# Optimization experiments

Measured on AMD Instinct MI355X. Metric: run time of the kernel, lower is better.

The kernel has to match this reference:

```python
import jax, jax.numpy as jnp
import numpy as np

B, N, DIM = 64, 512, 256
H, DH = 8, 64
INNER = H * DH
SCALE = DH ** -0.5


def setup_inputs() -> dict:
    key = jax.random.key(0)
    ks = jax.random.split(key, 8)
    x = jax.random.normal(ks[0], (B, N, DIM), dtype=jnp.float32)
    mask = jax.random.bernoulli(ks[1], 0.9, (B, N))
    attn_bias = jax.random.normal(ks[2], (1, H, N, N), dtype=jnp.float32)
    # weights stored [in, out] (torch Linear applies x @ W.T; here W = W_torch.T)
    Wq = jax.random.normal(ks[3], (DIM, INNER), dtype=jnp.float32) * (DIM ** -0.5)
    Wkv = jax.random.normal(ks[4], (DIM, 2 * INNER), dtype=jnp.float32) * (DIM ** -0.5)
    Wo = jax.random.normal(ks[5], (INNER, DIM), dtype=jnp.float32) * (INNER ** -0.5)
    bo = jnp.zeros((DIM,), dtype=jnp.float32)
    # gating linear: torch init is weight=0, bias=1 (gates==1); use small random
    # perturbation around that so the gate path is exercised numerically
    Wg = jax.random.normal(ks[6], (DIM, INNER), dtype=jnp.float32) * 0.02
    bg = jnp.ones((INNER,), dtype=jnp.float32)
    return {"x": x, "mask": mask, "attn_bias": attn_bias,
            "Wq": Wq, "Wkv": Wkv, "Wo": Wo, "bo": bo, "Wg": Wg, "bg": bg}


def reference(x, mask, attn_bias, Wq, Wkv, Wo, bo, Wg, bg):
    b, n, _ = x.shape
    # projections (no bias on q/kv, per nn.Linear(..., bias=False))
    q = x @ Wq                               # [b, n, H*DH]
    kv = x @ Wkv                             # [b, n, 2*H*DH]
    k, v = jnp.split(kv, 2, axis=-1)
    split_heads = lambda t: t.reshape(b, n, H, DH).transpose(0, 2, 1, 3)  # b h n d
    q, k, v = split_heads(q), split_heads(k), split_heads(v)
    dots = jnp.einsum('bhid,bhjd->bhij', q, k) * SCALE + attn_bias
    pair_mask = mask[:, None, :, None] & mask[:, None, None, :]  # [b,1,i,j]
    mask_value = -jnp.finfo(dots.dtype).max
    dots = jnp.where(pair_mask, dots, mask_value)
    attn = jax.nn.softmax(dots, axis=-1)
    out = jnp.einsum('bhij,bhjd->bhid', attn, v)
    out = out.transpose(0, 2, 1, 3).reshape(b, n, INNER)  # b n (h d)
    gates = x @ Wg + bg                      # note: no sigmoid in the original
    out = out * gates
    return out @ Wo + bo
```

## Files before the change

kernel.cpp:

```cpp
#include <hip/hip_runtime.h>
#include <stdint.h>

#define B_    64
#define N_    512
#define DIM_  256
#define H_    8
#define DH_   64
#define INNER_ 512

typedef __attribute__((ext_vector_type(8))) short bf16x8;
typedef __attribute__((ext_vector_type(4))) float f32x4;
typedef __attribute__((ext_vector_type(4))) short s16x4;

typedef const __attribute__((address_space(1))) void* gas_ptr;
typedef __attribute__((address_space(3))) void* las_ptr;

__device__ __forceinline__ short f2bf(float f) {
  unsigned int u = __float_as_uint(f);
  u += 0x7fffu + ((u >> 16) & 1u);
  return (short)(u >> 16);
}
__device__ __forceinline__ float bf2f(short s) {
  return __uint_as_float(((unsigned int)(unsigned short)s) << 16);
}
__device__ __forceinline__ void cp16(const void* g, void* l) {
  __builtin_amdgcn_global_load_lds((gas_ptr)g, (las_ptr)l, 16, 0, 0);
}
__device__ __forceinline__ f32x4 mfma16(bf16x8 a, bf16x8 b, f32x4 c) {
  return __builtin_amdgcn_mfma_f32_16x16x32_bf16(a, b, c, 0, 0, 0);
}

#define PREP_WT1  (2048 * 256)
#define PREP_WOT  (256 * 512)
#define PREP_X    (32768 * 256)
#define PREP_BIAS (8 * 512 * 512)
#define PREP_MASK (64 * 512)
#define PREP_TOT  (PREP_WT1 + PREP_WOT + PREP_X + PREP_BIAS + PREP_MASK)

__global__ void prep_k(const float* __restrict__ x,
                       const float* __restrict__ Wq, const float* __restrict__ Wkv,
                       const float* __restrict__ Wg, const float* __restrict__ Wo,
                       const float* __restrict__ bias, const int* __restrict__ mask,
                       short* __restrict__ Wt1, short* __restrict__ WoT,
                       short* __restrict__ xb, float* __restrict__ biasS,
                       float* __restrict__ maskF)
{
  const int idx = blockIdx.x * 256 + threadIdx.x;
  if (idx < PREP_WT1) {
    const int n = idx >> 8, k = idx & 255;
    float v;
    if (n < 512)        v = Wq[k * 512 + n];
    else if (n < 1536)  v = Wkv[k * 1024 + (n - 512)];
    else                v = Wg[k * 512 + (n - 1536)];
    Wt1[idx] = f2bf(v);
  } else if (idx < PREP_WT1 + PREP_WOT) {
    const int j = idx - PREP_WT1;
    const int n = j >> 9, k = j & 511;
    WoT[j] = f2bf(Wo[k * 256 + n]);
  } else if (idx < PREP_WT1 + PREP_WOT + PREP_X) {
    const int j = idx - (PREP_WT1 + PREP_WOT);
    xb[j] = f2bf(x[j]);
  } else if (idx < PREP_WT1 + PREP_WOT + PREP_X + PREP_BIAS) {
    const int j = idx - (PREP_WT1 + PREP_WOT + PREP_X);
    biasS[j] = bias[j] * 1.4426950408889634f;
  } else if (idx < PREP_TOT) {
    const int j = idx - (PREP_WT1 + PREP_WOT + PREP_X + PREP_BIAS);
    maskF[j] = mask[j] ? 1.0f : 0.0f;
  }
}

__global__ __launch_bounds__(256, 2) void gemm_qkvg(
    const short* __restrict__ X, const short* __restrict__ Wt,
    const float* __restrict__ bg,
    short* __restrict__ Q, short* __restrict__ Kb,
    short* __restrict__ Vt, short* __restrict__ G)
{
  __shared__ __align__(16) short As[128 * 32];
  __shared__ __align__(16) short Bs[128 * 32];
  const int tid = threadIdx.x;
  const int w = tid >> 6, lane = tid & 63;
  const int m = lane & 15, q = lane >> 4;
  const int n0 = blockIdx.x * 128, m0 = blockIdx.y * 128;
  const int region = blockIdx.x >> 2;
  const bool vreg = (region == 2);
  const int ric = lane >> 2, cslot = lane & 3;
  const int csw = cslot ^ ((ric >> 1) & 3);
  const int wr = (w >> 1) * 64, wc = (w & 1) * 64;
  const int rsw = (m >> 1) & 3;
  f32x4 acc[4][4] = {};
  for (int k0 = 0; k0 < DIM_; k0 += 32) {
    __syncthreads();
#pragma unroll
    for (int s = 0; s < 2; ++s) {
      const int rr = w * 32 + s * 16;
      cp16(X  + (size_t)(m0 + rr + ric) * DIM_ + (k0 + csw * 8), &As[rr * 32]);
      cp16(Wt + (size_t)(n0 + rr + ric) * DIM_ + (k0 + csw * 8), &Bs[rr * 32]);
    }
    __syncthreads();
    bf16x8 af[4], bfv[4];
#pragma unroll
    for (int t = 0; t < 4; ++t) {
      af[t]  = *(const bf16x8*)&As[(wr + t * 16 + m) * 32 + ((q ^ rsw) * 8)];
      bfv[t] = *(const bf16x8*)&Bs[(wc + t * 16 + m) * 32 + ((q ^ rsw) * 8)];
    }
    if (vreg) {
#pragma unroll
      for (int ti = 0; ti < 4; ++ti)
#pragma unroll
        for (int tj = 0; tj < 4; ++tj)
          acc[ti][tj] = mfma16(af[ti], bfv[tj], acc[ti][tj]);
    } else {
#pragma unroll
      for (int ti = 0; ti < 4; ++ti)
#pragma unroll
        for (int tj = 0; tj < 4; ++tj)
          acc[ti][tj] = mfma16(bfv[tj], af[ti], acc[ti][tj]);
    }
  }
  if (vreg) {
    const int cb = (n0 & 511) + wc;
#pragma unroll
    for (int ti = 0; ti < 4; ++ti) {
      const int mgb = m0 + wr + ti * 16 + q * 4;
      const int b = mgb >> 9, n = mgb & 511;
#pragma unroll
      for (int tj = 0; tj < 4; ++tj) {
        const int c = cb + tj * 16 + m;
        const int h = c >> 6, d = c & 63;
        s16x4 st;
#pragma unroll
        for (int r = 0; r < 4; ++r) st[r] = f2bf(acc[ti][tj][r]);
        *(s16x4*)&Vt[((size_t)(b * 8 + h) * 64 + d) * 512 + n] = st;
      }
    }
  } else {
#pragma unroll
    for (int ti = 0; ti < 4; ++ti) {
      const int xrow = m0 + wr + ti * 16 + m;
      const int b = xrow >> 9, n = xrow & 511;
#pragma unroll
      for (int tj = 0; tj < 4; ++tj) {
        const int cvec = (n0 & 511) + wc + tj * 16 + q * 4;
        if (region == 3) {
          const f32x4 bg4 = *(const f32x4*)&bg[cvec];
          s16x4 st;
#pragma unroll
          for (int r = 0; r < 4; ++r) st[r] = f2bf(acc[ti][tj][r] + bg4[r]);
          *(s16x4*)&G[(size_t)xrow * 512 + cvec] = st;
        } else {
          const int h = cvec >> 6, d0 = cvec & 63;
          s16x4 st;
#pragma unroll
          for (int r = 0; r < 4; ++r) st[r] = f2bf(acc[ti][tj][r]);
          short* dst = (region == 0) ? Q : Kb;
          *(s16x4*)&dst[((size_t)(b * 8 + h) * 512 + n) * 64 + d0] = st;
        }
      }
    }
  }
}

__global__ __launch_bounds__(256, 4) void attn_k(
    const short* __restrict__ Q, const short* __restrict__ K,
    const short* __restrict__ Vt, const float* __restrict__ biasS,
    const float* __restrict__ maskF, short* __restrict__ G)
{
  __shared__ __align__(16) short Ks[2][32 * 64];
  __shared__ __align__(16) short Vs[2][64 * 32];
  __shared__ __align__(16) short Pall[4][16 * 32];
  const int tid = threadIdx.x;
  const int w = tid >> 6, lane = tid & 63;
  const int m = lane & 15, q = lane >> 4;
  const int m7 = m & 7;
  const int vsw = (m ^ (m >> 2)) & 3;
  const int h = blockIdx.x, iq = blockIdx.y, b = blockIdx.z;
  const int i0w = iq * 128 + w * 32;
  const size_t bh = (size_t)b * 8 + h;
  const short* Qp = Q + (bh * 512 + i0w) * 64;
  const short* Kp = K + bh * 512 * 64;
  const short* Vp = Vt + bh * 64 * 512;
  const float* mkp = maskF + b * 512;
  short* Ps = Pall[w];

  const int srow = lane >> 3;
  const int gchunk = (lane & 7) ^ srow;
  const int vrow = lane >> 2;
  const int gchunkV = (lane & 3) ^ ((vrow ^ (vrow >> 2)) & 3);

  bf16x8 qf[2][2];
#pragma unroll
  for (int it = 0; it < 2; ++it) {
    qf[it][0] = *(const bf16x8*)&Qp[(it * 16 + m) * 64 + q * 8];
    qf[it][1] = *(const bf16x8*)&Qp[(it * 16 + m) * 64 + 32 + q * 8];
  }
  float miF[2];
#pragma unroll
  for (int it = 0; it < 2; ++it) miF[it] = mkp[i0w + it * 16 + m];

  cp16(Kp + (size_t)(w * 8 + srow) * 64 + gchunk * 8, &Ks[0][w * 8 * 64]);
  cp16(Vp + (size_t)(w * 16 + vrow) * 512 + gchunkV * 8, &Vs[0][w * 16 * 32]);

  f32x4 o[2][4] = {};
  float l[2] = {0.f, 0.f};
  __syncthreads();

  const float SCL = 0.125f * 1.4426950408889634f;
  for (int c = 0; c < 16; ++c) {
    const int p = c & 1;
    if (c < 15) {
      const int jn = (c + 1) * 32;
      cp16(Kp + (size_t)(jn + w * 8 + srow) * 64 + gchunk * 8, &Ks[p ^ 1][w * 8 * 64]);
      cp16(Vp + (size_t)(w * 16 + vrow) * 512 + jn + gchunkV * 8, &Vs[p ^ 1][w * 16 * 32]);
    }
    f32x4 mjf[2];
#pragma unroll
    for (int jt = 0; jt < 2; ++jt)
      mjf[jt] = *(const f32x4*)&mkp[c * 32 + jt * 16 + q * 4];

    f32x4 s[2][2];
    __builtin_amdgcn_s_setprio(1);
#pragma unroll
    for (int jt = 0; jt < 2; ++jt) {
      const bf16x8 ka = *(const bf16x8*)&Ks[p][(jt * 16 + m) * 64 + ((q ^ m7) * 8)];
      const bf16x8 kb = *(const bf16x8*)&Ks[p][(jt * 16 + m) * 64 + (((4 + q) ^ m7) * 8)];
#pragma unroll
      for (int it = 0; it < 2; ++it) {
        f32x4 a = {};
        a = mfma16(ka, qf[it][0], a);
        s[it][jt] = mfma16(kb, qf[it][1], a);
      }
    }
    __builtin_amdgcn_s_setprio(0);
#pragma unroll
    for (int it = 0; it < 2; ++it) {
      const float* bp = biasS + ((size_t)h * 512 + i0w + it * 16 + m) * 512 + c * 32;
      f32x4 bv[2];
#pragma unroll
      for (int jt = 0; jt < 2; ++jt)
        bv[jt] = *(const f32x4*)&bp[jt * 16 + q * 4];
#pragma unroll
      for (int jt = 0; jt < 2; ++jt) {
        s16x4 st;
#pragma unroll
        for (int r = 0; r < 4; ++r) {
          const float v = fmaf(s[it][jt][r], SCL, bv[jt][r]);
          float e = exp2f(v) * mjf[jt][r];
          e = (miF[it] != 0.0f) ? e : 1.0f;
          const unsigned u = __float_as_uint(e);
          st[r] = (short)(u >> 16);
          l[it] += __uint_as_float(u & 0xffff0000u);
        }
        *(s16x4*)&Ps[m * 32 + (((jt * 2 + (q >> 1)) ^ vsw) * 8) + (q & 1) * 4] = st;
      }
      const bf16x8 pa = *(const bf16x8*)&Ps[m * 32 + ((q ^ vsw) * 8)];
      __builtin_amdgcn_s_setprio(1);
#pragma unroll
      for (int dt = 0; dt < 4; ++dt) {
        const bf16x8 va = *(const bf16x8*)&Vs[p][(dt * 16 + m) * 32 + ((q ^ vsw) * 8)];
        o[it][dt] = mfma16(pa, va, o[it][dt]);
      }
      __builtin_amdgcn_s_setprio(0);
    }
    __syncthreads();
  }

#pragma unroll
  for (int it = 0; it < 2; ++it) {
    float t = l[it];
    t += __shfl_xor(t, 16, 64);
    t += __shfl_xor(t, 32, 64);
    l[it] = 1.0f / t;
  }
  const int colb = h * 64;
#pragma unroll
  for (int it = 0; it < 2; ++it) {
    float lr[4];
#pragma unroll
    for (int r = 0; r < 4; ++r) lr[r] = __shfl(l[it], q * 4 + r, 16);
#pragma unroll
    for (int dt = 0; dt < 4; ++dt)
#pragma unroll
      for (int r = 0; r < 4; ++r) {
        const int row = i0w + it * 16 + q * 4 + r;
        const size_t addr = ((size_t)b * 512 + row) * 512 + colb + dt * 16 + m;
        const float gate = bf2f(G[addr]);
        G[addr] = f2bf(o[it][dt][r] * lr[r] * gate);
      }
  }
}

__global__ __launch_bounds__(256, 2) void gemm_og(
    const short* __restrict__ A, const short* __restrict__ Bt,
    const float* __restrict__ bo, float* __restrict__ out)
{
  __shared__ __align__(16) short As[64 * 32];
  __shared__ __align__(16) short Bs[128 * 32];
  const int tid = threadIdx.x;
  const int w = tid >> 6, lane = tid & 63;
  const int m = lane & 15, q = lane >> 4;
  const int n0 = blockIdx.x * 128, m0 = blockIdx.y * 64;
  const int ric = lane >> 2, cslot = lane & 3;
  const int csw = cslot ^ ((ric >> 1) & 3);
  const int wr = (w >> 1) * 32, wc = (w & 1) * 64;
  const int rsw = (m >> 1) & 3;
  f32x4 acc[2][4] = {};
  for (int k0 = 0; k0 < INNER_; k0 += 32) {
    __syncthreads();
    cp16(A + (size_t)(m0 + w * 16 + ric) * INNER_ + (k0 + csw * 8), &As[w * 16 * 32]);
#pragma unroll
    for (int s = 0; s < 2; ++s) {
      const int rr = w * 32 + s * 16;
      cp16(Bt + (size_t)(n0 + rr + ric) * INNER_ + (k0 + csw * 8), &Bs[rr * 32]);
    }
    __syncthreads();
    bf16x8 af[2], bfv[4];
#pragma unroll
    for (int t = 0; t < 2; ++t)
      af[t]  = *(const bf16x8*)&As[(wr + t * 16 + m) * 32 + ((q ^ rsw) * 8)];
#pragma unroll
    for (int t = 0; t < 4; ++t)
      bfv[t] = *(const bf16x8*)&Bs[(wc + t * 16 + m) * 32 + ((q ^ rsw) * 8)];
#pragma unroll
    for (int ti = 0; ti < 2; ++ti)
#pragma unroll
      for (int tj = 0; tj < 4; ++tj)
        acc[ti][tj] = mfma16(bfv[tj], af[ti], acc[ti][tj]);
  }
#pragma unroll
  for (int ti = 0; ti < 2; ++ti) {
    const int row = m0 + wr + ti * 16 + m;
#pragma unroll
    for (int tj = 0; tj < 4; ++tj) {
      const int c0 = n0 + wc + tj * 16 + q * 4;
      const f32x4 bo4 = *(const f32x4*)&bo[c0];
      f32x4 v;
#pragma unroll
      for (int r = 0; r < 4; ++r) v[r] = acc[ti][tj][r] + bo4[r];
      *(f32x4*)&out[(size_t)row * 256 + c0] = v;
    }
  }
}

extern "C" void kernel_launch(void* const* d_in, const int* in_sizes, int n_in,
                              void* d_out, int out_size, void* d_ws, size_t ws_size,
                              hipStream_t stream)
{
  (void)in_sizes; (void)n_in; (void)out_size; (void)ws_size;
  const float* x    = (const float*)d_in[0];
  const int*   mask = (const int*)d_in[1];
  const float* bias = (const float*)d_in[2];
  const float* Wq   = (const float*)d_in[3];
  const float* Wkv  = (const float*)d_in[4];
  const float* Wo   = (const float*)d_in[5];
  const float* bo   = (const float*)d_in[6];
  const float* Wg   = (const float*)d_in[7];
  const float* bg   = (const float*)d_in[8];
  float* out = (float*)d_out;

  char* ws = (char*)d_ws;
  size_t off = 0;
  short* Wt1   = (short*)(ws + off); off += (size_t)2048 * 256 * 2;
  short* WoT   = (short*)(ws + off); off += (size_t)256 * 512 * 2;
  short* xb    = (short*)(ws + off); off += (size_t)32768 * 256 * 2;
  short* Qb    = (short*)(ws + off); off += (size_t)B_ * H_ * N_ * DH_ * 2;
  short* Kb    = (short*)(ws + off); off += (size_t)B_ * H_ * N_ * DH_ * 2;
  short* Vt    = (short*)(ws + off); off += (size_t)B_ * H_ * DH_ * N_ * 2;
  short* G     = (short*)(ws + off); off += (size_t)B_ * N_ * INNER_ * 2;
  float* biasS = (float*)(ws + off); off += (size_t)H_ * N_ * N_ * 4;
  float* maskF = (float*)(ws + off); off += (size_t)B_ * N_ * 4;

  prep_k<<<(PREP_TOT + 255) / 256, 256, 0, stream>>>(x, Wq, Wkv, Wg, Wo, bias, mask,
                                                     Wt1, WoT, xb, biasS, maskF);
  gemm_qkvg<<<dim3(16, 256), 256, 0, stream>>>(xb, Wt1, bg, Qb, Kb, Vt, G);
  attn_k<<<dim3(8, 4, 64), 256, 0, stream>>>(Qb, Kb, Vt, biasS, maskF, G);
  gemm_og<<<dim3(2, 512), 256, 0, stream>>>(G, WoT, bo, out);
}
```

Baseline: 307.8 us.

## Deepen attention K/V prefetch to a 4-slot ring with vmcnt waits

Replaces the double-buffered K/V LDS staging in the attention kernel with a 4-slot ring that prefetches two tiles ahead. Each iteration waits with an explicit vmcnt count plus a single barrier instead of a full __syncthreads at the end. The goal is to hide more global-load latency and cut one barrier per iteration. The cost is doubled K/V LDS use, which may lower occupancy. The manual vmcnt counting also has to stay in step with the other global loads in the loop, such as the mask and bias loads.

Measured after the change: 308.7 us. About the same (+0.3%).

```diff
diff --git a/kernel.cpp b/kernel.cpp
--- a/kernel.cpp
+++ b/kernel.cpp
@@ -29,6 +29,11 @@
 __device__ __forceinline__ f32x4 mfma16(bf16x8 a, bf16x8 b, f32x4 c) {
   return __builtin_amdgcn_mfma_f32_16x16x32_bf16(a, b, c, 0, 0, 0);
 }
+
+#define WAITVM(N) do { \
+  asm volatile("s_waitcnt vmcnt(" #N ")" ::: "memory"); \
+  __builtin_amdgcn_sched_barrier(0); \
+} while (0)
 
 #define PREP_WT1  (2048 * 256)
 #define PREP_WOT  (256 * 512)
@@ -165,8 +170,8 @@
     const short* __restrict__ Vt, const float* __restrict__ biasS,
     const float* __restrict__ maskF, short* __restrict__ G)
 {
-  __shared__ __align__(16) short Ks[2][32 * 64];
-  __shared__ __align__(16) short Vs[2][64 * 32];
+  __shared__ __align__(16) short Ks[4][32 * 64];
+  __shared__ __align__(16) short Vs[4][64 * 32];
   __shared__ __align__(16) short Pall[4][16 * 32];
   const int tid = threadIdx.x;
   const int w = tid >> 6, lane = tid & 63;
@@ -187,6 +192,12 @@
   const int vrow = lane >> 2;
   const int gchunkV = (lane & 3) ^ ((vrow ^ (vrow >> 2)) & 3);
 
+  auto STAGE = [&](int t) {
+    const int jn = t * 32;
+    cp16(Kp + (size_t)(jn + w * 8 + srow) * 64 + gchunk * 8, &Ks[t & 3][w * 8 * 64]);
+    cp16(Vp + (size_t)(w * 16 + vrow) * 512 + jn + gchunkV * 8, &Vs[t & 3][w * 16 * 32]);
+  };
+
   bf16x8 qf[2][2];
 #pragma unroll
   for (int it = 0; it < 2; ++it) {
@@ -197,21 +208,16 @@
 #pragma unroll
   for (int it = 0; it < 2; ++it) miF[it] = mkp[i0w + it * 16 + m];
 
-  cp16(Kp + (size_t)(w * 8 + srow) * 64 + gchunk * 8, &Ks[0][w * 8 * 64]);
-  cp16(Vp + (size_t)(w * 16 + vrow) * 512 + gchunkV * 8, &Vs[0][w * 16 * 32]);
+  STAGE(0);
+  STAGE(1);
 
   f32x4 o[2][4] = {};
   float l[2] = {0.f, 0.f};
-  __syncthreads();
 
   const float SCL = 0.125f * 1.4426950408889634f;
-  for (int c = 0; c < 16; ++c) {
-    const int p = c & 1;
-    if (c < 15) {
-      const int jn = (c + 1) * 32;
-      cp16(Kp + (size_t)(jn + w * 8 + srow) * 64 + gchunk * 8, &Ks[p ^ 1][w * 8 * 64]);
-      cp16(Vp + (size_t)(w * 16 + vrow) * 512 + jn + gchunkV * 8, &Vs[p ^ 1][w * 16 * 32]);
-    }
+
+  auto compute = [&](int c) {
+    const int p = c & 3;
     f32x4 mjf[2];
 #pragma unroll
     for (int jt = 0; jt < 2; ++jt)
@@ -261,8 +267,20 @@
       }
       __builtin_amdgcn_s_setprio(0);
     }
-    __syncthreads();
-  }
+  };
+
+  for (int c = 0; c < 14; ++c) {
+    STAGE(c + 2);
+    WAITVM(4);
+    __builtin_amdgcn_s_barrier();
+    compute(c);
+  }
+  WAITVM(2);
+  __builtin_amdgcn_s_barrier();
+  compute(14);
+  WAITVM(0);
+  __builtin_amdgcn_s_barrier();
+  compute(15);
 
 #pragma unroll
   for (int it = 0; it < 2; ++it) {
```
